# Kernel optimization log

Hardware: AMD Instinct MI355X
Metric: run time of the kernel (lower is better)

## Reference

```python
import jax, jax.numpy as jnp
import numpy as np

B, S, D, H = 4, 2048, 1024, 16


def setup_inputs() -> dict:
    key = jax.random.key(0)
    ks = jax.random.split(key, 5)
    scale = 1.0 / np.sqrt(D)
    return {
        "q": jax.random.normal(ks[0], (B, S, D), jnp.float32),
        "v": jax.random.normal(ks[1], (B, S, D), jnp.float32),
        "Wq": jax.random.normal(ks[2], (D, D), jnp.float32) * scale,
        "bq": jnp.zeros((D,), jnp.float32),
        "Wk": jax.random.normal(ks[3], (D, D), jnp.float32) * scale,
        "bk": jnp.zeros((D,), jnp.float32),
        "Wv": jax.random.normal(ks[4], (D, D), jnp.float32) * scale,
        "bv": jnp.zeros((D,), jnp.float32),
    }


def reference(q, v, Wq, bq, Wk, bk, Wv, bv):
    # k defaults to v in the original call
    k = v
    embed_dim = Wq.shape[0]
    num_heads = H
    dh = embed_dim // num_heads
    b, s, _ = q.shape

    qp = q @ Wq + bq  # [B,S,D]
    kp = k @ Wk + bk
    vp = v @ Wv + bv

    # tf.split(x, H, axis=2) + concat on axis 0 == reshape to [B,S,H,dh]
    qh = qp.reshape(b, s, num_heads, dh)
    kh = kp.reshape(b, s, num_heads, dh)
    vh = vp.reshape(b, s, num_heads, dh)

    # NOTE: original scales by sqrt(embed_dim), NOT sqrt(head_dim)
    scores = jnp.einsum("bqhd,bkhd->bhqk", qh, kh) / jnp.sqrt(
        jnp.asarray(embed_dim, qh.dtype)
    )
    att = jax.nn.softmax(scores, axis=-1)
    out = jnp.einsum("bhqk,bkhd->bqhd", att, vh)
    return out.reshape(b, s, embed_dim)
```

## Files before the change

### kernel.cpp

```cpp
#include <hip/hip_runtime.h>
#include <hip/hip_bf16.h>
#include <math.h>

#define B_   4
#define S_   2048
#define D_   1024
#define H_   16
#define DH_  64
#define M_   (B_ * S_)
#define BH_  (B_ * H_)

typedef __bf16 bf16x8_t __attribute__((ext_vector_type(8)));
typedef float  f32x4_t  __attribute__((ext_vector_type(4)));
typedef float  f32x16_t __attribute__((ext_vector_type(16)));

#define QSCALE 0.045084220027780106f

__device__ __forceinline__ unsigned short f2bf(float x) {
  unsigned int u = __float_as_uint(x);
  u += 0x7fffu + ((u >> 16) & 1u);
  return (unsigned short)(u >> 16);
}

__device__ __forceinline__ unsigned int pk2(float lo, float hi) {
  return (unsigned int)f2bf(lo) | ((unsigned int)f2bf(hi) << 16);
}

__device__ __forceinline__ void async16(const void* g, void* l) {
  __builtin_amdgcn_global_load_lds(
      (__attribute__((address_space(1))) unsigned int*)(void*)g,
      (__attribute__((address_space(3))) unsigned int*)l, 16, 0, 0);
}

__global__ __launch_bounds__(256) void cvt_f32_bf16(
    const float* __restrict__ q, const float* __restrict__ v,
    unsigned short* __restrict__ qb, unsigned short* __restrict__ vb) {
  const float* src = blockIdx.y ? v : q;
  unsigned short* dst = blockIdx.y ? vb : qb;
  size_t i = ((size_t)blockIdx.x * 256 + threadIdx.x) * 4;
  float4 a = *(const float4*)(src + i);
  ushort4 o;
  o.x = f2bf(a.x); o.y = f2bf(a.y); o.z = f2bf(a.z); o.w = f2bf(a.w);
  *(ushort4*)(dst + i) = o;
}

__global__ void wtrans(const float* __restrict__ Wq, const float* __restrict__ Wk,
                       const float* __restrict__ Wv,
                       unsigned short* __restrict__ Wqt, unsigned short* __restrict__ Wkt,
                       unsigned short* __restrict__ Wvt) {
  int z = blockIdx.z;
  const float* W = (z == 0) ? Wq : (z == 1 ? Wk : Wv);
  unsigned short* Wt = (z == 0) ? Wqt : (z == 1 ? Wkt : Wvt);
  __shared__ float tile[32][33];
  int tx = threadIdx.x, ty = threadIdx.y;
  int n = blockIdx.x * 32 + tx;
#pragma unroll
  for (int i = 0; i < 4; ++i) {
    int k = blockIdx.y * 32 + ty + i * 8;
    tile[ty + i * 8][tx] = W[(size_t)k * D_ + n];
  }
  __syncthreads();
  int k2 = blockIdx.y * 32 + tx;
#pragma unroll
  for (int i = 0; i < 4; ++i) {
    int n2 = blockIdx.x * 32 + ty + i * 8;
    Wt[(size_t)n2 * D_ + k2] = f2bf(tile[tx][ty + i * 8]);
  }
}

__global__ __launch_bounds__(256) void proj_gemm(
    const unsigned short* __restrict__ Aq, const unsigned short* __restrict__ Av,
    const unsigned short* __restrict__ Wqt, const unsigned short* __restrict__ Wkt,
    const unsigned short* __restrict__ Wvt,
    const float* __restrict__ bq, const float* __restrict__ bk, const float* __restrict__ bv,
    unsigned short* __restrict__ qp, unsigned short* __restrict__ kp,
    unsigned short* __restrict__ vt) {
  int z = blockIdx.z;
  const unsigned short* A  = (z == 0) ? Aq : Av;
  const unsigned short* Wt = (z == 0) ? Wqt : (z == 1 ? Wkt : Wvt);
  const float* bias        = (z == 0) ? bq : (z == 1 ? bk : bv);
  unsigned short* outp     = (z == 0) ? qp : (z == 1 ? kp : vt);
  const float cs           = (z == 0) ? QSCALE : 1.0f;

  __shared__ __attribute__((aligned(16))) unsigned short Alds[128 * 32];
  __shared__ __attribute__((aligned(16))) unsigned short Blds[128 * 32];

  int t = threadIdx.x;
  int lane = t & 63, wave = t >> 6;
  int lrow = lane & 15, lq = lane >> 4;
  int wm = (wave & 1) * 64, wn = (wave >> 1) * 64;
  int m0 = blockIdx.y * 128, n0 = blockIdx.x * 128;

  f32x4_t acc[4][4];
#pragma unroll
  for (int i = 0; i < 4; ++i)
#pragma unroll
    for (int j = 0; j < 4; ++j) acc[i][j] = (f32x4_t){0.f, 0.f, 0.f, 0.f};

  for (int k0 = 0; k0 < D_; k0 += 32) {
    __syncthreads();
#pragma unroll
    for (int r = 0; r < 2; ++r) {
      int off = t * 16 + r * 4096;
      int row = off >> 6, slot = (off >> 4) & 3;
      int ch = (slot ^ (row >> 1)) & 3;
      async16((const char*)A  + ((size_t)(m0 + row) * D_ + k0) * 2 + ch * 16, (char*)Alds + off);
      async16((const char*)Wt + ((size_t)(n0 + row) * D_ + k0) * 2 + ch * 16, (char*)Blds + off);
    }
    __syncthreads();

    bf16x8_t af[4], bfr[4];
#pragma unroll
    for (int i = 0; i < 4; ++i) {
      int ra = wm + i * 16 + lrow;
      int rb = wn + i * 16 + lrow;
      af[i]  = *(const bf16x8_t*)(Alds + ra * 32 + ((lq ^ (ra >> 1)) & 3) * 8);
      bfr[i] = *(const bf16x8_t*)(Blds + rb * 32 + ((lq ^ (rb >> 1)) & 3) * 8);
    }
#pragma unroll
    for (int i = 0; i < 4; ++i)
#pragma unroll
      for (int j = 0; j < 4; ++j)
        acc[i][j] = __builtin_amdgcn_mfma_f32_16x16x32_bf16(af[i], bfr[j], acc[i][j], 0, 0, 0);
  }

#pragma unroll
  for (int j = 0; j < 4; ++j) {
    int n = n0 + wn + j * 16 + lrow;
    float bv_ = bias[n];
    int h = n >> 6, d = n & 63;
#pragma unroll
    for (int i = 0; i < 4; ++i) {
      int mbase = m0 + wm + i * 16 + lq * 4;
      int b = mbase >> 11, s = mbase & 2047;
      if (z != 2) {
#pragma unroll
        for (int r = 0; r < 4; ++r)
          outp[(((size_t)(b * H_ + h) * S_ + (s + r)) << 6) + d] = f2bf((acc[i][j][r] + bv_) * cs);
      } else {
        ushort4 pk;
        pk.x = f2bf(acc[i][j][0] + bv_);
        pk.y = f2bf(acc[i][j][1] + bv_);
        pk.z = f2bf(acc[i][j][2] + bv_);
        pk.w = f2bf(acc[i][j][3] + bv_);
        *(ushort4*)(outp + (((size_t)(b * H_ + h) * 64 + d) << 11) + s) = pk;
      }
    }
  }
}

__global__ __launch_bounds__(256, 2) void attn(
    const unsigned short* __restrict__ qp, const unsigned short* __restrict__ kp,
    const unsigned short* __restrict__ vt, float* __restrict__ out) {
  const int qt = blockIdx.x;
  const int bh = blockIdx.y;
  const int t = threadIdx.x;
  const int lane = t & 63, wave = t >> 6;
  const int h = lane >> 5, ln = lane & 31;

  __shared__ __attribute__((aligned(16))) unsigned short Klds[64 * 64];
  __shared__ __attribute__((aligned(16))) unsigned short Vlds[64 * 64];

  const int q0 = qt * 256 + wave * 64;

  bf16x8_t qf[2][4];
#pragma unroll
  for (int rt = 0; rt < 2; ++rt)
#pragma unroll
    for (int ks = 0; ks < 4; ++ks)
      qf[rt][ks] = *(const bf16x8_t*)(qp + ((size_t)bh * S_ + q0 + rt * 32 + ln) * 64 + ks * 16 + h * 8);

  f32x16_t o[2][2];
  float l[2] = {0.f, 0.f};
#pragma unroll
  for (int rt = 0; rt < 2; ++rt)
#pragma unroll
    for (int dt = 0; dt < 2; ++dt)
#pragma unroll
      for (int r = 0; r < 16; ++r) o[rt][dt][r] = 0.f;

  const unsigned short* kg = kp + (size_t)bh * S_ * 64;
  const unsigned short* vg = vt + (size_t)bh * 64 * S_;

  for (int kb = 0; kb < S_; kb += 64) {
    __syncthreads();
#pragma unroll
    for (int r = 0; r < 2; ++r) {
      int off = t * 16 + r * 4096;
      int row = off >> 7, slot = (off >> 4) & 7;
      int ch = slot ^ (row & 7);
      async16((const char*)kg + ((size_t)(kb + row)) * 128 + ch * 16, (char*)Klds + off);
      async16((const char*)vg + ((size_t)row * S_ + kb) * 2 + ch * 16, (char*)Vlds + off);
    }
    __syncthreads();

    f32x16_t st[2][2];
#pragma unroll
    for (int rt = 0; rt < 2; ++rt)
#pragma unroll
      for (int kt = 0; kt < 2; ++kt)
#pragma unroll
        for (int r = 0; r < 16; ++r) st[rt][kt][r] = 0.f;
#pragma unroll
    for (int kt = 0; kt < 2; ++kt)
#pragma unroll
      for (int ks = 0; ks < 4; ++ks) {
        int row = kt * 32 + ln;
        bf16x8_t kf = *(const bf16x8_t*)(Klds + row * 64 + (((ks * 2 + h) ^ (row & 7)) * 8));
#pragma unroll
        for (int rt = 0; rt < 2; ++rt)
          st[rt][kt] = __builtin_amdgcn_mfma_f32_32x32x16_bf16(kf, qf[rt][ks], st[rt][kt], 0, 0, 0);
      }

    unsigned int pkv[2][2][8];
#pragma unroll
    for (int rt = 0; rt < 2; ++rt) {
      float lp = 0.f;
#pragma unroll
      for (int kt = 0; kt < 2; ++kt)
#pragma unroll
        for (int i = 0; i < 8; ++i) {
          float p0 = exp2f(st[rt][kt][2 * i]);
          float p1 = exp2f(st[rt][kt][2 * i + 1]);
          lp += p0 + p1;
          pkv[rt][kt][i] = pk2(p0, p1);
        }
      l[rt] += lp + __shfl_xor(lp, 32);
    }

    bf16x8_t pf[2][4];
#pragma unroll
    for (int rt = 0; rt < 2; ++rt)
#pragma unroll
      for (int ks = 0; ks < 4; ++ks) {
        int kt = ks >> 1, b = 4 * (ks & 1);
        unsigned int e0 = __shfl_xor(h ? pkv[rt][kt][b]     : pkv[rt][kt][b + 2], 32);
        unsigned int e1 = __shfl_xor(h ? pkv[rt][kt][b + 1] : pkv[rt][kt][b + 3], 32);
        union { unsigned int u[4]; bf16x8_t v; } fr;
        fr.u[0] = h ? e0 : pkv[rt][kt][b];
        fr.u[1] = h ? e1 : pkv[rt][kt][b + 1];
        fr.u[2] = h ? pkv[rt][kt][b + 2] : e0;
        fr.u[3] = h ? pkv[rt][kt][b + 3] : e1;
        pf[rt][ks] = fr.v;
      }

#pragma unroll
    for (int dt = 0; dt < 2; ++dt)
#pragma unroll
      for (int ks = 0; ks < 4; ++ks) {
        int row = dt * 32 + ln;
        bf16x8_t vf = *(const bf16x8_t*)(Vlds + row * 64 + (((ks * 2 + h) ^ (row & 7)) * 8));
#pragma unroll
        for (int rt = 0; rt < 2; ++rt)
          o[rt][dt] = __builtin_amdgcn_mfma_f32_32x32x16_bf16(pf[rt][ks], vf, o[rt][dt], 0, 0, 0);
      }
  }

  const int b = bh >> 4, head = bh & 15;
#pragma unroll
  for (int rt = 0; rt < 2; ++rt)
#pragma unroll
    for (int r = 0; r < 16; ++r) {
      int rowl = (r & 3) + 8 * (r >> 2) + 4 * h;
      float li = __shfl(l[rt], rowl, 64);
      float inv = 1.0f / li;
      int rg = q0 + rt * 32 + rowl;
      float* op = out + ((size_t)b * S_ + rg) * D_ + head * 64 + ln;
      op[0]  = o[rt][0][r] * inv;
      op[32] = o[rt][1][r] * inv;
    }
}

extern "C" void kernel_launch(void* const* d_in, const int* in_sizes, int n_in,
                              void* d_out, int out_size, void* d_ws, size_t ws_size,
                              hipStream_t stream) {
  const float* q  = (const float*)d_in[0];
  const float* v  = (const float*)d_in[1];
  const float* Wq = (const float*)d_in[2];
  const float* bq = (const float*)d_in[3];
  const float* Wk = (const float*)d_in[4];
  const float* bk = (const float*)d_in[5];
  const float* Wv = (const float*)d_in[6];
  const float* bv = (const float*)d_in[7];
  float* out = (float*)d_out;

  char* ws = (char*)d_ws;
  unsigned short* qb  = (unsigned short*)(ws);
  unsigned short* vb  = (unsigned short*)(ws + (16u << 20));
  unsigned short* Wqt = (unsigned short*)(ws + (32u << 20));
  unsigned short* Wkt = (unsigned short*)(ws + (34u << 20));
  unsigned short* Wvt = (unsigned short*)(ws + (36u << 20));
  unsigned short* qpp = (unsigned short*)(ws + (38u << 20));
  unsigned short* kpp = (unsigned short*)(ws + (54u << 20));
  unsigned short* vtp = (unsigned short*)(ws + (70u << 20));

  hipLaunchKernelGGL(cvt_f32_bf16, dim3((M_ * D_) / 1024, 2), dim3(256), 0, stream,
                     q, v, qb, vb);
  hipLaunchKernelGGL(wtrans, dim3(32, 32, 3), dim3(32, 8), 0, stream,
                     Wq, Wk, Wv, Wqt, Wkt, Wvt);
  hipLaunchKernelGGL(proj_gemm, dim3(D_ / 128, M_ / 128, 3), dim3(256), 0, stream,
                     qb, vb, Wqt, Wkt, Wvt, bq, bk, bv, qpp, kpp, vtp);
  hipLaunchKernelGGL(attn, dim3(S_ / 256, BH_), dim3(256), 0, stream,
                     qpp, kpp, vtp, out);
}
```

Before: 337.5 us.

## Double-buffer attention K/V tiles, remap grids for XCD locality, cheaper exp/pack

```diff
diff --git a/kernel.cpp b/kernel.cpp
--- a/kernel.cpp
+++ b/kernel.cpp
@@ -22,8 +22,8 @@
   return (unsigned short)(u >> 16);
 }
 
-__device__ __forceinline__ unsigned int pk2(float lo, float hi) {
-  return (unsigned int)f2bf(lo) | ((unsigned int)f2bf(hi) << 16);
+__device__ __forceinline__ unsigned int pk2t(float lo, float hi) {
+  return __builtin_amdgcn_perm(__float_as_uint(hi), __float_as_uint(lo), 0x07060302u);
 }
 
 __device__ __forceinline__ void async16(const void* g, void* l) {
@@ -75,13 +75,18 @@
     const float* __restrict__ bq, const float* __restrict__ bk, const float* __restrict__ bv,
     unsigned short* __restrict__ qp, unsigned short* __restrict__ kp,
     unsigned short* __restrict__ vt) {
-  int z = blockIdx.z;
+  int z = blockIdx.y;
   const unsigned short* A  = (z == 0) ? Aq : Av;
   const unsigned short* Wt = (z == 0) ? Wqt : (z == 1 ? Wkt : Wvt);
   const float* bias        = (z == 0) ? bq : (z == 1 ? bk : bv);
   unsigned short* outp     = (z == 0) ? qp : (z == 1 ? kp : vt);
   const float cs           = (z == 0) ? QSCALE : 1.0f;
 
+  int lin = blockIdx.x;
+  int xcd = lin & 7, j = lin >> 3;
+  int m0 = (xcd * 8 + (j & 7)) * 128;
+  int n0 = (j >> 3) * 128;
+
   __shared__ __attribute__((aligned(16))) unsigned short Alds[128 * 32];
   __shared__ __attribute__((aligned(16))) unsigned short Blds[128 * 32];
 
@@ -89,13 +94,12 @@
   int lane = t & 63, wave = t >> 6;
   int lrow = lane & 15, lq = lane >> 4;
   int wm = (wave & 1) * 64, wn = (wave >> 1) * 64;
-  int m0 = blockIdx.y * 128, n0 = blockIdx.x * 128;
 
   f32x4_t acc[4][4];
 #pragma unroll
   for (int i = 0; i < 4; ++i)
 #pragma unroll
-    for (int j = 0; j < 4; ++j) acc[i][j] = (f32x4_t){0.f, 0.f, 0.f, 0.f};
+    for (int j2 = 0; j2 < 4; ++j2) acc[i][j2] = (f32x4_t){0.f, 0.f, 0.f, 0.f};
 
   for (int k0 = 0; k0 < D_; k0 += 32) {
     __syncthreads();
@@ -120,13 +124,13 @@
 #pragma unroll
     for (int i = 0; i < 4; ++i)
 #pragma unroll
-      for (int j = 0; j < 4; ++j)
-        acc[i][j] = __builtin_amdgcn_mfma_f32_16x16x32_bf16(af[i], bfr[j], acc[i][j], 0, 0, 0);
-  }
-
-#pragma unroll
-  for (int j = 0; j < 4; ++j) {
-    int n = n0 + wn + j * 16 + lrow;
+      for (int j2 = 0; j2 < 4; ++j2)
+        acc[i][j2] = __builtin_amdgcn_mfma_f32_16x16x32_bf16(af[i], bfr[j2], acc[i][j2], 0, 0, 0);
+  }
+
+#pragma unroll
+  for (int j2 = 0; j2 < 4; ++j2) {
+    int n = n0 + wn + j2 * 16 + lrow;
     float bv_ = bias[n];
     int h = n >> 6, d = n & 63;
 #pragma unroll
@@ -136,13 +140,13 @@
       if (z != 2) {
 #pragma unroll
         for (int r = 0; r < 4; ++r)
-          outp[(((size_t)(b * H_ + h) * S_ + (s + r)) << 6) + d] = f2bf((acc[i][j][r] + bv_) * cs);
+          outp[(((size_t)(b * H_ + h) * S_ + (s + r)) << 6) + d] = f2bf((acc[i][j2][r] + bv_) * cs);
       } else {
         ushort4 pk;
-        pk.x = f2bf(acc[i][j][0] + bv_);
-        pk.y = f2bf(acc[i][j][1] + bv_);
-        pk.z = f2bf(acc[i][j][2] + bv_);
-        pk.w = f2bf(acc[i][j][3] + bv_);
+        pk.x = f2bf(acc[i][j2][0] + bv_);
+        pk.y = f2bf(acc[i][j2][1] + bv_);
+        pk.z = f2bf(acc[i][j2][2] + bv_);
+        pk.w = f2bf(acc[i][j2][3] + bv_);
         *(ushort4*)(outp + (((size_t)(b * H_ + h) * 64 + d) << 11) + s) = pk;
       }
     }
@@ -152,14 +156,14 @@
 __global__ __launch_bounds__(256, 2) void attn(
     const unsigned short* __restrict__ qp, const unsigned short* __restrict__ kp,
     const unsigned short* __restrict__ vt, float* __restrict__ out) {
-  const int qt = blockIdx.x;
-  const int bh = blockIdx.y;
+  const int bh = blockIdx.x;
+  const int qt = blockIdx.y;
   const int t = threadIdx.x;
   const int lane = t & 63, wave = t >> 6;
   const int h = lane >> 5, ln = lane & 31;
 
-  __shared__ __attribute__((aligned(16))) unsigned short Klds[64 * 64];
-  __shared__ __attribute__((aligned(16))) unsigned short Vlds[64 * 64];
+  __shared__ __attribute__((aligned(16))) unsigned short Klds[2][64 * 64];
+  __shared__ __attribute__((aligned(16))) unsigned short Vlds[2][64 * 64];
 
   const int q0 = qt * 256 + wave * 64;
 
@@ -179,38 +183,52 @@
 #pragma unroll
       for (int r = 0; r < 16; ++r) o[rt][dt][r] = 0.f;
 
+  f32x16_t z16;
+#pragma unroll
+  for (int r = 0; r < 16; ++r) z16[r] = 0.f;
+
   const unsigned short* kg = kp + (size_t)bh * S_ * 64;
   const unsigned short* vg = vt + (size_t)bh * 64 * S_;
 
-  for (int kb = 0; kb < S_; kb += 64) {
-    __syncthreads();
+  auto stage = [&](int kb, int bi) {
 #pragma unroll
     for (int r = 0; r < 2; ++r) {
       int off = t * 16 + r * 4096;
       int row = off >> 7, slot = (off >> 4) & 7;
       int ch = slot ^ (row & 7);
-      async16((const char*)kg + ((size_t)(kb + row)) * 128 + ch * 16, (char*)Klds + off);
-      async16((const char*)vg + ((size_t)row * S_ + kb) * 2 + ch * 16, (char*)Vlds + off);
-    }
+      async16((const char*)(kg + (size_t)(kb + row) * 64 + ch * 8), (char*)&Klds[bi][0] + off);
+      async16((const char*)(vg + (size_t)row * S_ + kb + ch * 8), (char*)&Vlds[bi][0] + off);
+    }
+  };
+
+  stage(0, 0);
+
+  const int NT = S_ / 64;
+  for (int it = 0; it < NT; ++it) {
+    const int bi = it & 1;
     __syncthreads();
+    if (it + 1 < NT) stage((it + 1) * 64, bi ^ 1);
+
+    const unsigned short* Kb = &Klds[bi][0];
+    const unsigned short* Vb = &Vlds[bi][0];
 
     f32x16_t st[2][2];
 #pragma unroll
-    for (int rt = 0; rt < 2; ++rt)
-#pragma unroll
-      for (int kt = 0; kt < 2; ++kt)
-#pragma unroll
-        for (int r = 0; r < 16; ++r) st[rt][kt][r] = 0.f;
-#pragma unroll
-    for (int kt = 0; kt < 2; ++kt)
-#pragma unroll
-      for (int ks = 0; ks < 4; ++ks) {
+    for (int kt = 0; kt < 2; ++kt) {
+      {
         int row = kt * 32 + ln;
-        bf16x8_t kf = *(const bf16x8_t*)(Klds + row * 64 + (((ks * 2 + h) ^ (row & 7)) * 8));
-#pragma unroll
-        for (int rt = 0; rt < 2; ++rt)
-          st[rt][kt] = __builtin_amdgcn_mfma_f32_32x32x16_bf16(kf, qf[rt][ks], st[rt][kt], 0, 0, 0);
-      }
+        bf16x8_t kf = *(const bf16x8_t*)(Kb + row * 64 + (((0 + h) ^ (row & 7)) * 8));
+        st[0][kt] = __builtin_amdgcn_mfma_f32_32x32x16_bf16(kf, qf[0][0], z16, 0, 0, 0);
+        st[1][kt] = __builtin_amdgcn_mfma_f32_32x32x16_bf16(kf, qf[1][0], z16, 0, 0, 0);
+      }
+#pragma unroll
+      for (int ks = 1; ks < 4; ++ks) {
+        int row = kt * 32 + ln;
+        bf16x8_t kf = *(const bf16x8_t*)(Kb + row * 64 + (((ks * 2 + h) ^ (row & 7)) * 8));
+        st[0][kt] = __builtin_amdgcn_mfma_f32_32x32x16_bf16(kf, qf[0][ks], st[0][kt], 0, 0, 0);
+        st[1][kt] = __builtin_amdgcn_mfma_f32_32x32x16_bf16(kf, qf[1][ks], st[1][kt], 0, 0, 0);
+      }
+    }
 
     unsigned int pkv[2][2][8];
 #pragma unroll
@@ -220,10 +238,10 @@
       for (int kt = 0; kt < 2; ++kt)
 #pragma unroll
         for (int i = 0; i < 8; ++i) {
-          float p0 = exp2f(st[rt][kt][2 * i]);
-          float p1 = exp2f(st[rt][kt][2 * i + 1]);
+          float p0 = __builtin_amdgcn_exp2f(st[rt][kt][2 * i]);
+          float p1 = __builtin_amdgcn_exp2f(st[rt][kt][2 * i + 1]);
           lp += p0 + p1;
-          pkv[rt][kt][i] = pk2(p0, p1);
+          pkv[rt][kt][i] = pk2t(p0, p1);
         }
       l[rt] += lp + __shfl_xor(lp, 32);
     }
@@ -249,7 +267,7 @@
 #pragma unroll
       for (int ks = 0; ks < 4; ++ks) {
         int row = dt * 32 + ln;
-        bf16x8_t vf = *(const bf16x8_t*)(Vlds + row * 64 + (((ks * 2 + h) ^ (row & 7)) * 8));
+        bf16x8_t vf = *(const bf16x8_t*)(Vb + row * 64 + (((ks * 2 + h) ^ (row & 7)) * 8));
 #pragma unroll
         for (int rt = 0; rt < 2; ++rt)
           o[rt][dt] = __builtin_amdgcn_mfma_f32_32x32x16_bf16(pf[rt][ks], vf, o[rt][dt], 0, 0, 0);
@@ -263,7 +281,7 @@
     for (int r = 0; r < 16; ++r) {
       int rowl = (r & 3) + 8 * (r >> 2) + 4 * h;
       float li = __shfl(l[rt], rowl, 64);
-      float inv = 1.0f / li;
+      float inv = __builtin_amdgcn_rcpf(li);
       int rg = q0 + rt * 32 + rowl;
       float* op = out + ((size_t)b * S_ + rg) * D_ + head * 64 + ln;
       op[0]  = o[rt][0][r] * inv;
@@ -298,8 +316,8 @@
                      q, v, qb, vb);
   hipLaunchKernelGGL(wtrans, dim3(32, 32, 3), dim3(32, 8), 0, stream,
                      Wq, Wk, Wv, Wqt, Wkt, Wvt);
-  hipLaunchKernelGGL(proj_gemm, dim3(D_ / 128, M_ / 128, 3), dim3(256), 0, stream,
+  hipLaunchKernelGGL(proj_gemm, dim3(512, 3), dim3(256), 0, stream,
                      qb, vb, Wqt, Wkt, Wvt, bq, bk, bv, qpp, kpp, vtp);
-  hipLaunchKernelGGL(attn, dim3(S_ / 256, BH_), dim3(256), 0, stream,
+  hipLaunchKernelGGL(attn, dim3(BH_, S_ / 256), dim3(256), 0, stream,
                      qpp, kpp, vtp, out);
 }
```

Result: faster. 274.3 us (-18.7%).
